# Optimization experiments

Measured on AMD Instinct MI355X. Metric: run time of the kernel, lower is better.

The kernel has to match this reference:

```python
import jax, jax.numpy as jnp
import numpy as np

D_MODEL = 1024
N_HEADS = 16
HEAD_DIM = D_MODEL // N_HEADS


def setup_inputs() -> dict:
    key = jax.random.key(0)
    ks = jax.random.split(key, 5)
    B, T = 4, 4096
    x = jax.random.normal(ks[0], (B, T, D_MODEL), dtype=jnp.float32)
    s = 1.0 / np.sqrt(D_MODEL)
    Wqkv = jax.random.normal(ks[1], (D_MODEL, 3 * D_MODEL), dtype=jnp.float32) * s
    bqkv = jnp.zeros((3 * D_MODEL,), dtype=jnp.float32)
    Wout = jax.random.normal(ks[2], (D_MODEL, D_MODEL), dtype=jnp.float32) * s
    bout = jnp.zeros((D_MODEL,), dtype=jnp.float32)
    return {"x": x, "Wqkv": Wqkv, "bqkv": bqkv, "Wout": Wout, "bout": bout}


def _feature_map(x):
    # elu(x) + 1  (strictly positive feature map)
    return jax.nn.elu(x) + 1.0


def reference(x, Wqkv, bqkv, Wout, bout):
    B, T, C = x.shape
    H, D = N_HEADS, HEAD_DIM
    qkv = x @ Wqkv + bqkv                      # [B,T,3C]
    qkv = qkv.reshape(B, T, 3, H, D)
    qkv = jnp.transpose(qkv, (2, 0, 3, 1, 4))  # [3,B,H,T,D]
    q, k, v = qkv[0], qkv[1], qkv[2]
    scale = D ** 0.25
    q_m = _feature_map(q / scale)
    k_m = _feature_map(k / scale)
    kv = jnp.einsum('bhtd,bhtm->bhdm', k_m, v)     # [B,H,D,D]
    out = jnp.einsum('bhtd,bhdm->bhtm', q_m, kv)   # [B,H,T,D]
    z = q_m.sum(axis=-1, keepdims=True)            # note: sum over feature dim (as in source)
    out = out / (z + 1e-6)
    out = jnp.transpose(out, (0, 2, 1, 3)).reshape(B, T, C)
    return out @ Wout + bout
```

## Files before the change

### kernel.cpp

```cpp
#include <hip/hip_runtime.h>
#include <hip/hip_bf16.h>
#include <math.h>

#define B_ 4
#define T_ 4096
#define H_ 16
#define D_ 64
#define C_ 1024
#define BT_ (B_*T_)

using short8  = __attribute__((ext_vector_type(8))) short;
using floatx4 = __attribute__((ext_vector_type(4))) float;

__device__ __forceinline__ float feature_map(float x) {
    return x > 0.0f ? x + 1.0f : __expf(x);
}
__device__ __forceinline__ unsigned short f2bf(float x) {
    union { __hip_bfloat16 b; unsigned short u; } c;
    c.b = __float2bfloat16(x);
    return c.u;
}
__device__ __forceinline__ float bf2f(unsigned short u) {
    union { unsigned int u; float f; } c;
    c.u = (unsigned)u << 16;
    return c.f;
}
__device__ __forceinline__ void async16(const void* g, void* l) {
    __builtin_amdgcn_global_load_lds(
        (const __attribute__((address_space(1))) void*)g,
        (__attribute__((address_space(3))) void*)l, 16, 0, 0);
}
__device__ __forceinline__ const char* sel3(const char* a0, const char* a1,
                                            const char* a2, int t) {
    return t == 0 ? a0 : (t == 1 ? a1 : a2);
}

__global__ __launch_bounds__(256)
void convert_x_kernel(const float4* __restrict__ x, ushort* __restrict__ xb)
{
    const size_t i = ((size_t)blockIdx.x * 256 + threadIdx.x) * 2;
    const float4 a = x[i], b = x[i + 1];
    short8 r;
    r[0] = (short)f2bf(a.x); r[1] = (short)f2bf(a.y);
    r[2] = (short)f2bf(a.z); r[3] = (short)f2bf(a.w);
    r[4] = (short)f2bf(b.x); r[5] = (short)f2bf(b.y);
    r[6] = (short)f2bf(b.z); r[7] = (short)f2bf(b.w);
    *reinterpret_cast<short8*>(&xb[i * 4]) = r;
}

__global__ __launch_bounds__(256)
void transpose_bf16_kernel(const float* __restrict__ W, ushort* __restrict__ WT,
                           int K, int N)
{
    __shared__ float t[32][33];
    const int n0 = blockIdx.x * 32, k0 = blockIdx.y * 32;
    const int r = threadIdx.x >> 5, c = threadIdx.x & 31;
    #pragma unroll
    for (int i = 0; i < 4; i++)
        t[r + 8 * i][c] = W[(size_t)(k0 + r + 8 * i) * N + n0 + c];
    __syncthreads();
    #pragma unroll
    for (int i = 0; i < 4; i++)
        WT[(size_t)(n0 + r + 8 * i) * K + k0 + c] = f2bf(t[c][r + 8 * i]);
}

#define BAR()    __builtin_amdgcn_s_barrier()
#define WAITDS() do { asm volatile("s_waitcnt lgkmcnt(0)" ::: "memory"); \
                      __builtin_amdgcn_sched_barrier(0); } while(0)
#define VM6()    do { asm volatile("s_waitcnt vmcnt(6)" ::: "memory"); \
                      __builtin_amdgcn_sched_barrier(0); } while(0)

#define LDA(slot, mf, ks, buf) \
    aR[slot][ks] = *(const short8*)(smem + (buf)*32768 + ((mf)>>2)*16384 + \
                                    aRowB + ((mf)&3)*2048 + cks##ks)
#define LDB(nf, ks, buf) \
    bR[nf][ks] = *(const short8*)(smem + 65536 + (buf)*32768 + ((nf)>>1)*16384 + \
                                  bRowB + ((nf)&1)*2048 + cks##ks)
#define LDA8(MB, BUF) do { \
    LDA(0, MB+0, 0, BUF); LDA(0, MB+0, 1, BUF); \
    LDA(1, MB+1, 0, BUF); LDA(1, MB+1, 1, BUF); \
    LDA(2, MB+2, 0, BUF); LDA(2, MB+2, 1, BUF); \
    LDA(3, MB+3, 0, BUF); LDA(3, MB+3, 1, BUF); } while(0)
#define LDB4(NF, BUF) do { \
    LDB(NF+0, 0, BUF); LDB(NF+0, 1, BUF); \
    LDB(NF+1, 0, BUF); LDB(NF+1, 1, BUF); } while(0)

#define MM(mf, nf, ks, slot) \
    acc[mf][nf] = __builtin_amdgcn_mfma_f32_16x16x32_bf16( \
        aR[slot][ks], bR[nf][ks], acc[mf][nf], 0, 0, 0)
#define MFMAQ(MB, NF) do { \
    MM(MB+0,NF+0,0,0); MM(MB+1,NF+0,0,1); MM(MB+2,NF+0,0,2); MM(MB+3,NF+0,0,3); \
    MM(MB+0,NF+1,0,0); MM(MB+1,NF+1,0,1); MM(MB+2,NF+1,0,2); MM(MB+3,NF+1,0,3); \
    MM(MB+0,NF+0,1,0); MM(MB+1,NF+0,1,1); MM(MB+2,NF+0,1,2); MM(MB+3,NF+0,1,3); \
    MM(MB+0,NF+1,1,0); MM(MB+1,NF+1,1,1); MM(MB+2,NF+1,1,2); MM(MB+3,NF+1,1,3); \
} while(0)

#define STGA(h, G, buf) do { int _g = (G); if (_g >= NTILE*16) _g -= NTILE*16; \
    const char* _b = sel3(Ab0, Ab1, Ab2, _g >> 4); const int _w = (_g & 15) * 128; \
    async16(_b + aOf##h##0 + _w, smem + (buf)*32768 + (h)*16384 + wv*1024); \
    async16(_b + aOf##h##1 + _w, smem + (buf)*32768 + (h)*16384 + 8192 + wv*1024); \
} while(0)
#define STGB(h, G, buf) do { int _g = (G); if (_g >= NTILE*16) _g -= NTILE*16; \
    const char* _b = sel3(Bb0, Bb1, Bb2, _g >> 4); const int _w = (_g & 15) * 128; \
    async16(_b + bOf##h##0 + _w, smem + 65536 + (buf)*32768 + (h)*16384 + wv*1024); \
    async16(_b + bOf##h##1 + _w, smem + 65536 + (buf)*32768 + (h)*16384 + 8192 + wv*1024); \
} while(0)

#define ITERBODY(GB) \
    const int g1 = (GB) + 2*it + 1, g2 = (GB) + 2*it + 2, g3 = (GB) + 2*it + 3; \
     LDA8(0, 0); LDB4(0, 0); STGA(1, g1, 1); \
    BAR(); WAITDS(); __builtin_amdgcn_s_setprio(1); MFMAQ(0, 0); \
    __builtin_amdgcn_s_setprio(0); BAR(); \
     LDB4(2, 0); STGA(0, g2, 0); \
    BAR(); WAITDS(); __builtin_amdgcn_s_setprio(1); MFMAQ(0, 2); \
    __builtin_amdgcn_s_setprio(0); BAR(); \
     LDA8(4, 0); STGB(0, g2, 0); \
    BAR(); WAITDS(); __builtin_amdgcn_s_setprio(1); MFMAQ(4, 2); \
    __builtin_amdgcn_s_setprio(0); BAR(); \
     STGB(1, g2, 0); \
    BAR(); WAITDS(); __builtin_amdgcn_s_setprio(1); MFMAQ(4, 0); \
    __builtin_amdgcn_s_setprio(0); VM6(); BAR(); \
     LDA8(0, 1); LDB4(0, 1); STGA(1, g2, 0); \
    BAR(); WAITDS(); __builtin_amdgcn_s_setprio(1); MFMAQ(0, 0); \
    __builtin_amdgcn_s_setprio(0); BAR(); \
     LDB4(2, 1); STGA(0, g3, 1); \
    BAR(); WAITDS(); __builtin_amdgcn_s_setprio(1); MFMAQ(0, 2); \
    __builtin_amdgcn_s_setprio(0); BAR(); \
     LDA8(4, 1); STGB(0, g3, 1); \
    BAR(); WAITDS(); __builtin_amdgcn_s_setprio(1); MFMAQ(4, 2); \
    __builtin_amdgcn_s_setprio(0); BAR(); \
     STGB(1, g3, 1); \
    BAR(); WAITDS(); __builtin_amdgcn_s_setprio(1); MFMAQ(4, 0); \
    __builtin_amdgcn_s_setprio(0); VM6(); BAR();

template<int EPI>
__device__ __forceinline__ void gemm_epilogue(
    floatx4 (&acc)[8][4], const float (&bv)[4],
    int mBase, int nBase, int wm, int wn, int lr, int quad,
    ushort* __restrict__ q_out, ushort* __restrict__ kT_out,
    ushort* __restrict__ vT_out, float* __restrict__ f_out)
{
    if (EPI == 0) {
        const float inv_scale = 0.35355339059327373f;
        const int seg = nBase >> 10;
        if (seg == 0) {
            #pragma unroll
            for (int nf = 0; nf < 4; nf++) {
                const int c = nBase + wn * 64 + nf * 16 + lr;
                #pragma unroll
                for (int mf = 0; mf < 8; mf++)
                    #pragma unroll
                    for (int i = 0; i < 4; i++) {
                        const int t = mBase + wm * 128 + mf * 16 + quad * 4 + i;
                        q_out[(size_t)t * C_ + c] =
                            f2bf(feature_map((acc[mf][nf][i] + bv[nf]) * inv_scale));
                    }
            }
        } else {
            ushort* dstT = (seg == 1) ? kT_out : vT_out;
            #pragma unroll
            for (int nf = 0; nf < 4; nf++) {
                const int c = (nBase + wn * 64 + nf * 16 + lr) & 1023;
                #pragma unroll
                for (int mf = 0; mf < 8; mf++) {
                    float v0 = acc[mf][nf][0] + bv[nf], v1 = acc[mf][nf][1] + bv[nf];
                    float v2 = acc[mf][nf][2] + bv[nf], v3 = acc[mf][nf][3] + bv[nf];
                    if (seg == 1) {
                        v0 = feature_map(v0 * inv_scale); v1 = feature_map(v1 * inv_scale);
                        v2 = feature_map(v2 * inv_scale); v3 = feature_map(v3 * inv_scale);
                    }
                    const int tt = mBase + wm * 128 + mf * 16 + quad * 4;
                    *(ushort4*)&dstT[(size_t)c * BT_ + tt] =
                        make_ushort4(f2bf(v0), f2bf(v1), f2bf(v2), f2bf(v3));
                }
            }
        }
    } else {
        #pragma unroll
        for (int nf = 0; nf < 4; nf++) {
            const int c = nBase + wn * 64 + nf * 16 + lr;
            #pragma unroll
            for (int mf = 0; mf < 8; mf++)
                #pragma unroll
                for (int i = 0; i < 4; i++) {
                    const int row = mBase + wm * 128 + mf * 16 + quad * 4 + i;
                    f_out[(size_t)row * C_ + c] = acc[mf][nf][i] + bv[nf];
                }
        }
    }
    #pragma unroll
    for (int i = 0; i < 8; i++)
        #pragma unroll
        for (int j = 0; j < 4; j++) acc[i][j] = (floatx4)0.0f;
}

template<int EPI, int NBX, int NTILE>
__global__ __launch_bounds__(512, 2)
void gemm256_8ph(const ushort* __restrict__ A, const ushort* __restrict__ Bm,
                 const float* __restrict__ bias,
                 ushort* __restrict__ q_out, ushort* __restrict__ kT_out,
                 ushort* __restrict__ vT_out, float* __restrict__ f_out)
{
    __shared__ __align__(16) unsigned char smem[131072];

    const int tid = threadIdx.x;
    const int wv = tid >> 6, l = tid & 63;
    const int wm = wv >> 2, wn = wv & 3;
    const int lr = l & 15, quad = l >> 4;

    int mB0, mB1, mB2, nB0, nB1, nB2;
    {
        const int tot = (int)gridDim.x * NTILE, cpx = tot >> 3;
        int lg0 = blockIdx.x;
        int w0 = (lg0 & 7) * cpx + (lg0 >> 3);
        mB0 = (w0 / NBX) * 256; nB0 = (w0 % NBX) * 256;
        if (NTILE > 1) {
            int lg1 = blockIdx.x + (int)gridDim.x;
            int w1 = (lg1 & 7) * cpx + (lg1 >> 3);
            mB1 = (w1 / NBX) * 256; nB1 = (w1 % NBX) * 256;
            int lg2 = blockIdx.x + 2 * (int)gridDim.x;
            int w2 = (lg2 & 7) * cpx + (lg2 >> 3);
            mB2 = (w2 / NBX) * 256; nB2 = (w2 % NBX) * 256;
        } else { mB1 = mB0; nB1 = nB0; mB2 = mB0; nB2 = nB0; }
    }
    const char* Ab0 = (const char*)(A + (size_t)mB0 * C_);
    const char* Ab1 = (const char*)(A + (size_t)mB1 * C_);
    const char* Ab2 = (const char*)(A + (size_t)mB2 * C_);
    const char* Bb0 = (const char*)(Bm + (size_t)nB0 * C_);
    const char* Bb1 = (const char*)(Bm + (size_t)nB1 * C_);
    const char* Bb2 = (const char*)(Bm + (size_t)nB2 * C_);

    float bv0[4], bv1[4], bv2[4];
    #pragma unroll
    for (int nf = 0; nf < 4; nf++) {
        bv0[nf] = bias[nB0 + wn * 64 + nf * 16 + lr];
        bv1[nf] = (NTILE > 1) ? bias[nB1 + wn * 64 + nf * 16 + lr] : bv0[nf];
        bv2[nf] = (NTILE > 1) ? bias[nB2 + wn * 64 + nf * 16 + lr] : bv0[nf];
    }

    const int s0 = tid >> 3;
    const int cb = ((tid & 7) * 16) ^ ((s0 & 7) << 4);
    const int aOf00 = (s0)       * 2048 + cb;
    const int aOf01 = (128 + s0) * 2048 + cb;
    const int aOf10 = (64 + s0)  * 2048 + cb;
    const int aOf11 = (192 + s0) * 2048 + cb;
    const int bq    = (s0 >> 5) * 64 + (s0 & 31);
    const int bOf00 = (bq)       * 2048 + cb;
    const int bOf01 = (bq + 128) * 2048 + cb;
    const int bOf10 = (bq + 32)  * 2048 + cb;
    const int bOf11 = (bq + 160) * 2048 + cb;

    const int aRowB = (wm * 64 + lr) * 128;
    const int bRowB = (wn * 32 + lr) * 128;
    const int cks0 = (quad * 16) ^ ((lr & 7) << 4);
    const int cks1 = 64 ^ cks0;

    floatx4 acc[8][4];
    #pragma unroll
    for (int i = 0; i < 8; i++)
        #pragma unroll
        for (int j = 0; j < 4; j++) acc[i][j] = (floatx4)0.0f;
    short8 aR[4][2], bR[4][2];

    STGA(0, 0, 0);
    STGB(0, 0, 0);
    STGB(1, 0, 0);
    STGA(1, 0, 0);
    STGA(0, 1, 1);
    STGB(0, 1, 1);
    STGB(1, 1, 1);
    asm volatile("s_waitcnt vmcnt(6)" ::: "memory");
    __builtin_amdgcn_sched_barrier(0);
    BAR();

    #pragma unroll 1
    for (int it = 0; it < 8; ++it) { ITERBODY(0) }
    gemm_epilogue<EPI>(acc, bv0, mB0, nB0, wm, wn, lr, quad,
                       q_out, kT_out, vT_out, f_out);
    if (NTILE > 1) {
        #pragma unroll 1
        for (int it = 0; it < 8; ++it) { ITERBODY(16) }
        gemm_epilogue<EPI>(acc, bv1, mB1, nB1, wm, wn, lr, quad,
                           q_out, kT_out, vT_out, f_out);
        #pragma unroll 1
        for (int it = 0; it < 8; ++it) { ITERBODY(32) }
        gemm_epilogue<EPI>(acc, bv2, mB2, nB2, wm, wn, lr, quad,
                           q_out, kT_out, vT_out, f_out);
    }
    asm volatile("s_waitcnt vmcnt(0)" ::: "memory");
}

__global__ __launch_bounds__(256)
void kv_accum_kernel(const ushort* __restrict__ kmT, const ushort* __restrict__ vT,
                     float* __restrict__ kv)
{
    const int tid = threadIdx.x;
    const int w = tid >> 6, l = tid & 63;
    const int wm = w >> 1, wn = w & 1;
    const int lr = l & 15, quad = l >> 4;
    const int bh = blockIdx.y;
    const int b = bh >> 4, h = bh & 15;
    const size_t t0 = (size_t)b * T_ + (size_t)blockIdx.x * 512;

    const ushort* Ar = kmT + (size_t)(h * 64 + wm * 32 + lr) * BT_ + t0 + quad * 8;
    const ushort* Br = vT  + (size_t)(h * 64 + wn * 32 + lr) * BT_ + t0 + quad * 8;

    floatx4 acc[2][2];
    #pragma unroll
    for (int i = 0; i < 2; i++)
        #pragma unroll
        for (int j = 0; j < 2; j++) acc[i][j] = (floatx4)0.0f;

    #pragma unroll 8
    for (int tt = 0; tt < 512; tt += 32) {
        const short8 af0 = *(const short8*)&Ar[tt];
        const short8 af1 = *(const short8*)&Ar[(size_t)16 * BT_ + tt];
        const short8 bf0 = *(const short8*)&Br[tt];
        const short8 bf1 = *(const short8*)&Br[(size_t)16 * BT_ + tt];
        acc[0][0] = __builtin_amdgcn_mfma_f32_16x16x32_bf16(af0, bf0, acc[0][0], 0, 0, 0);
        acc[0][1] = __builtin_amdgcn_mfma_f32_16x16x32_bf16(af0, bf1, acc[0][1], 0, 0, 0);
        acc[1][0] = __builtin_amdgcn_mfma_f32_16x16x32_bf16(af1, bf0, acc[1][0], 0, 0, 0);
        acc[1][1] = __builtin_amdgcn_mfma_f32_16x16x32_bf16(af1, bf1, acc[1][1], 0, 0, 0);
    }

    float* kvb = kv + (size_t)bh * (D_ * D_);
    #pragma unroll
    for (int i = 0; i < 2; i++)
        #pragma unroll
        for (int j = 0; j < 2; j++)
            #pragma unroll
            for (int r = 0; r < 4; r++) {
                const int d = wm * 32 + i * 16 + quad * 4 + r;
                const int m = wn * 32 + j * 16 + lr;
                atomicAdd(&kvb[d * 64 + m], acc[i][j][r]);
            }
}

__global__ __launch_bounds__(256)
void pv_kernel(const ushort* __restrict__ qm, const float* __restrict__ kv,
               ushort* __restrict__ attn)
{
    __shared__ ushort kvs[64 * 72];
    const int tid = threadIdx.x;
    const int w = tid >> 6, l = tid & 63;
    const int lr = l & 15, quad = l >> 4;
    const int h = blockIdx.x;
    const int tBase = blockIdx.y * 256;
    const int b = tBase >> 12;

    const float* kvg = kv + ((size_t)b * H_ + h) * (D_ * D_);
    #pragma unroll
    for (int e = 0; e < 4; e++) {
        const int flat = (e * 256 + tid) * 4;
        const float4 vv = *(const float4*)&kvg[flat];
        const int d = flat >> 6, m = flat & 63;
        kvs[(m + 0) * 72 + d] = f2bf(vv.x);
        kvs[(m + 1) * 72 + d] = f2bf(vv.y);
        kvs[(m + 2) * 72 + d] = f2bf(vv.z);
        kvs[(m + 3) * 72 + d] = f2bf(vv.w);
    }
    __syncthreads();

    const int tw = tBase + w * 64;

    floatx4 acc[4][4];
    #pragma unroll
    for (int i = 0; i < 4; i++)
        #pragma unroll
        for (int j = 0; j < 4; j++) acc[i][j] = (floatx4)0.0f;

    float zp[4] = {0.0f, 0.0f, 0.0f, 0.0f};

    #pragma unroll
    for (int kk = 0; kk < 2; kk++) {
        short8 bf[4];
        #pragma unroll
        for (int tf = 0; tf < 4; tf++) {
            bf[tf] = *(const short8*)&qm[(size_t)(tw + tf * 16 + lr) * C_
                                         + h * 64 + kk * 32 + quad * 8];
            #pragma unroll
            for (int j = 0; j < 8; j++) zp[tf] += bf2f((unsigned short)bf[tf][j]);
        }
        short8 af[4];
        #pragma unroll
        for (int mf = 0; mf < 4; mf++)
            af[mf] = *(const short8*)&kvs[(mf * 16 + lr) * 72 + kk * 32 + quad * 8];
        #pragma unroll
        for (int mf = 0; mf < 4; mf++)
            #pragma unroll
            for (int tf = 0; tf < 4; tf++)
                acc[mf][tf] = __builtin_amdgcn_mfma_f32_16x16x32_bf16(
                    af[mf], bf[tf], acc[mf][tf], 0, 0, 0);
    }

    #pragma unroll
    for (int tf = 0; tf < 4; tf++) {
        zp[tf] += __shfl_xor(zp[tf], 16);
        zp[tf] += __shfl_xor(zp[tf], 32);
    }

    #pragma unroll
    for (int tf = 0; tf < 4; tf++) {
        const int t = tw + tf * 16 + lr;
        const float inv = 1.0f / (zp[tf] + 1e-6f);
        #pragma unroll
        for (int mf = 0; mf < 4; mf++) {
            const int m = mf * 16 + quad * 4;
            *(ushort4*)&attn[(size_t)t * C_ + h * 64 + m] =
                make_ushort4(f2bf(acc[mf][tf][0] * inv), f2bf(acc[mf][tf][1] * inv),
                             f2bf(acc[mf][tf][2] * inv), f2bf(acc[mf][tf][3] * inv));
        }
    }
}

extern "C" void kernel_launch(void* const* d_in, const int* in_sizes, int n_in,
                              void* d_out, int out_size, void* d_ws, size_t ws_size,
                              hipStream_t stream)
{
    const float* x    = (const float*)d_in[0];
    const float* Wqkv = (const float*)d_in[1];
    const float* bqkv = (const float*)d_in[2];
    const float* Wout = (const float*)d_in[3];
    const float* bout = (const float*)d_in[4];
    float* out = (float*)d_out;

    char* ws = (char*)d_ws;
    ushort* xb     = (ushort*)ws;
    ushort* WqkvT  = (ushort*)(ws + 33554432);
    ushort* WoutT  = (ushort*)(ws + 39845888);
    ushort* vT     = (ushort*)(ws + 41943040);
    float*  kv     = (float*) (ws + 75497472);
    ushort* attn   = (ushort*)ws;
    ushort* qm     = (ushort*)d_out;
    ushort* kmT    = (ushort*)((char*)d_out + 33554432);

    hipMemsetAsync(kv, 0, (size_t)B_ * H_ * D_ * D_ * sizeof(float), stream);

    convert_x_kernel<<<(BT_ * C_ / 8) / 256, 256, 0, stream>>>((const float4*)x, xb);
    transpose_bf16_kernel<<<dim3(3 * C_ / 32, C_ / 32), 256, 0, stream>>>(Wqkv, WqkvT, C_, 3 * C_);
    transpose_bf16_kernel<<<dim3(C_ / 32, C_ / 32), 256, 0, stream>>>(Wout, WoutT, C_, C_);

    gemm256_8ph<0, 12, 3><<<dim3(256), 512, 0, stream>>>(
        xb, WqkvT, bqkv, qm, kmT, vT, nullptr);
    kv_accum_kernel<<<dim3(8, B_ * H_), 256, 0, stream>>>(kmT, vT, kv);
    pv_kernel<<<dim3(H_, BT_ / 256), 256, 0, stream>>>(qm, kv, attn);
    gemm256_8ph<1, 4, 1><<<dim3(256), 512, 0, stream>>>(
        attn, WoutT, bout, nullptr, nullptr, nullptr, out);
}
```

Baseline: 312.1 us.

## Fold KV state into output projection weights, drop separate attention pass

The normalizer z is computed and applied in the QKV GEMM epilogue, so q is stored pre-scaled. A small per-batch kernel then multiplies each head's KV matrix into Wout, giving a per-batch fused weight. The output GEMM uses q directly against that weight, which removes the pv_kernel and its full read and write of the attention activations. The cost is a per-batch 1024x1024 weight (4x the weight traffic in the out GEMM), extra shuffles in the epilogue, and bf16 rounding of the combined KV·Wout product. The x conversion kernel also switches to a grid-stride loop over 2048 blocks.

```diff
diff --git a/kernel.cpp b/kernel.cpp
--- a/kernel.cpp
+++ b/kernel.cpp
@@ -20,11 +20,6 @@
     c.b = __float2bfloat16(x);
     return c.u;
 }
-__device__ __forceinline__ float bf2f(unsigned short u) {
-    union { unsigned int u; float f; } c;
-    c.u = (unsigned)u << 16;
-    return c.f;
-}
 __device__ __forceinline__ void async16(const void* g, void* l) {
     __builtin_amdgcn_global_load_lds(
         (const __attribute__((address_space(1))) void*)g,
@@ -38,14 +33,17 @@
 __global__ __launch_bounds__(256)
 void convert_x_kernel(const float4* __restrict__ x, ushort* __restrict__ xb)
 {
-    const size_t i = ((size_t)blockIdx.x * 256 + threadIdx.x) * 2;
-    const float4 a = x[i], b = x[i + 1];
-    short8 r;
-    r[0] = (short)f2bf(a.x); r[1] = (short)f2bf(a.y);
-    r[2] = (short)f2bf(a.z); r[3] = (short)f2bf(a.w);
-    r[4] = (short)f2bf(b.x); r[5] = (short)f2bf(b.y);
-    r[6] = (short)f2bf(b.z); r[7] = (short)f2bf(b.w);
-    *reinterpret_cast<short8*>(&xb[i * 4]) = r;
+    const size_t n = (size_t)BT_ * C_ / 8;
+    for (size_t i = (size_t)blockIdx.x * 256 + threadIdx.x; i < n;
+         i += (size_t)2048 * 256) {
+        const float4 a = x[2 * i], b = x[2 * i + 1];
+        short8 r;
+        r[0] = (short)f2bf(a.x); r[1] = (short)f2bf(a.y);
+        r[2] = (short)f2bf(a.z); r[3] = (short)f2bf(a.w);
+        r[4] = (short)f2bf(b.x); r[5] = (short)f2bf(b.y);
+        r[6] = (short)f2bf(b.z); r[7] = (short)f2bf(b.w);
+        *reinterpret_cast<short8*>(&xb[i * 8]) = r;
+    }
 }
 
 __global__ __launch_bounds__(256)
@@ -145,17 +143,24 @@
         const int seg = nBase >> 10;
         if (seg == 0) {
             #pragma unroll
-            for (int nf = 0; nf < 4; nf++) {
-                const int c = nBase + wn * 64 + nf * 16 + lr;
+            for (int mf = 0; mf < 8; mf++)
                 #pragma unroll
-                for (int mf = 0; mf < 8; mf++)
-                    #pragma unroll
-                    for (int i = 0; i < 4; i++) {
-                        const int t = mBase + wm * 128 + mf * 16 + quad * 4 + i;
-                        q_out[(size_t)t * C_ + c] =
-                            f2bf(feature_map((acc[mf][nf][i] + bv[nf]) * inv_scale));
-                    }
-            }
+                for (int i = 0; i < 4; i++) {
+                    float f0 = feature_map((acc[mf][0][i] + bv[0]) * inv_scale);
+                    float f1 = feature_map((acc[mf][1][i] + bv[1]) * inv_scale);
+                    float f2 = feature_map((acc[mf][2][i] + bv[2]) * inv_scale);
+                    float f3 = feature_map((acc[mf][3][i] + bv[3]) * inv_scale);
+                    float z = f0 + f1 + f2 + f3;
+                    z += __shfl_xor(z, 1); z += __shfl_xor(z, 2);
+                    z += __shfl_xor(z, 4); z += __shfl_xor(z, 8);
+                    const float inv = 1.0f / (z + 1e-6f);
+                    const int t = mBase + wm * 128 + mf * 16 + quad * 4 + i;
+                    const int cbase = nBase + wn * 64 + lr;
+                    q_out[(size_t)t * C_ + cbase]      = f2bf(f0 * inv);
+                    q_out[(size_t)t * C_ + cbase + 16] = f2bf(f1 * inv);
+                    q_out[(size_t)t * C_ + cbase + 32] = f2bf(f2 * inv);
+                    q_out[(size_t)t * C_ + cbase + 48] = f2bf(f3 * inv);
+                }
         } else {
             ushort* dstT = (seg == 1) ? kT_out : vT_out;
             #pragma unroll
@@ -195,11 +200,11 @@
 }
 
 template<int EPI, int NBX, int NTILE>
-__global__ __launch_bounds__(512, 2)
-void gemm256_8ph(const ushort* __restrict__ A, const ushort* __restrict__ Bm,
-                 const float* __restrict__ bias,
-                 ushort* __restrict__ q_out, ushort* __restrict__ kT_out,
-                 ushort* __restrict__ vT_out, float* __restrict__ f_out)
+__device__ __forceinline__ void gemm_body(
+    const ushort* __restrict__ A, const ushort* __restrict__ Bm,
+    const float* __restrict__ bias,
+    ushort* __restrict__ q_out, ushort* __restrict__ kT_out,
+    ushort* __restrict__ vT_out, float* __restrict__ f_out)
 {
     __shared__ __align__(16) unsigned char smem[131072];
 
@@ -223,12 +228,13 @@
             mB2 = (w2 / NBX) * 256; nB2 = (w2 % NBX) * 256;
         } else { mB1 = mB0; nB1 = nB0; mB2 = mB0; nB2 = nB0; }
     }
+    const size_t bOffB = (EPI == 1) ? (size_t)(mB0 >> 12) * ((size_t)C_ * C_) : 0;
     const char* Ab0 = (const char*)(A + (size_t)mB0 * C_);
     const char* Ab1 = (const char*)(A + (size_t)mB1 * C_);
     const char* Ab2 = (const char*)(A + (size_t)mB2 * C_);
-    const char* Bb0 = (const char*)(Bm + (size_t)nB0 * C_);
-    const char* Bb1 = (const char*)(Bm + (size_t)nB1 * C_);
-    const char* Bb2 = (const char*)(Bm + (size_t)nB2 * C_);
+    const char* Bb0 = (const char*)(Bm + bOffB + (size_t)nB0 * C_);
+    const char* Bb1 = (const char*)(Bm + bOffB + (size_t)nB1 * C_);
+    const char* Bb2 = (const char*)(Bm + bOffB + (size_t)nB2 * C_);
 
     float bv0[4], bv1[4], bv2[4];
     #pragma unroll
@@ -262,13 +268,8 @@
         for (int j = 0; j < 4; j++) acc[i][j] = (floatx4)0.0f;
     short8 aR[4][2], bR[4][2];
 
-    STGA(0, 0, 0);
-    STGB(0, 0, 0);
-    STGB(1, 0, 0);
-    STGA(1, 0, 0);
-    STGA(0, 1, 1);
-    STGB(0, 1, 1);
-    STGB(1, 1, 1);
+    STGA(0, 0, 0); STGB(0, 0, 0); STGB(1, 0, 0); STGA(1, 0, 0);
+    STGA(0, 1, 1); STGB(0, 1, 1); STGB(1, 1, 1);
     asm volatile("s_waitcnt vmcnt(6)" ::: "memory");
     __builtin_amdgcn_sched_barrier(0);
     BAR();
@@ -290,6 +291,21 @@
     asm volatile("s_waitcnt vmcnt(0)" ::: "memory");
 }
 
+__global__ __launch_bounds__(512, 2)
+void qkv8_kernel(const ushort* __restrict__ A, const ushort* __restrict__ Bm,
+                 const float* __restrict__ bias, ushort* __restrict__ q_out,
+                 ushort* __restrict__ kT_out, ushort* __restrict__ vT_out)
+{
+    gemm_body<0, 12, 3>(A, Bm, bias, q_out, kT_out, vT_out, nullptr);
+}
+
+__global__ __launch_bounds__(512, 2)
+void outproj8_kernel(const ushort* __restrict__ A, const ushort* __restrict__ Bm,
+                     const float* __restrict__ bias, float* __restrict__ f_out)
+{
+    gemm_body<1, 4, 1>(A, Bm, bias, nullptr, nullptr, nullptr, f_out);
+}
+
 __global__ __launch_bounds__(256)
 void kv_accum_kernel(const ushort* __restrict__ kmT, const ushort* __restrict__ vT,
                      float* __restrict__ kv)
@@ -337,31 +353,32 @@
 }
 
 __global__ __launch_bounds__(256)
-void pv_kernel(const ushort* __restrict__ qm, const float* __restrict__ kv,
-               ushort* __restrict__ attn)
-{
-    __shared__ ushort kvs[64 * 72];
+void kw_kernel(const float* __restrict__ kv, const ushort* __restrict__ WoutT,
+               ushort* __restrict__ KWT)
+{
     const int tid = threadIdx.x;
     const int w = tid >> 6, l = tid & 63;
     const int lr = l & 15, quad = l >> 4;
-    const int h = blockIdx.x;
-    const int tBase = blockIdx.y * 256;
-    const int b = tBase >> 12;
-
-    const float* kvg = kv + ((size_t)b * H_ + h) * (D_ * D_);
-    #pragma unroll
-    for (int e = 0; e < 4; e++) {
-        const int flat = (e * 256 + tid) * 4;
-        const float4 vv = *(const float4*)&kvg[flat];
-        const int d = flat >> 6, m = flat & 63;
-        kvs[(m + 0) * 72 + d] = f2bf(vv.x);
-        kvs[(m + 1) * 72 + d] = f2bf(vv.y);
-        kvs[(m + 2) * 72 + d] = f2bf(vv.z);
-        kvs[(m + 3) * 72 + d] = f2bf(vv.w);
-    }
-    __syncthreads();
-
-    const int tw = tBase + w * 64;
+    const int bh = blockIdx.y, b = bh >> 4, h = bh & 15;
+    const int c0 = blockIdx.x * 256 + w * 64;
+
+    const float* kvb = kv + (size_t)bh * (D_ * D_);
+
+    short8 bf[4][2];
+    #pragma unroll
+    for (int df = 0; df < 4; df++)
+        #pragma unroll
+        for (int ks = 0; ks < 2; ks++) {
+            const float* src = &kvb[(df * 16 + lr) * 64 + ks * 32 + quad * 8];
+            const float4 u0 = *(const float4*)src;
+            const float4 u1 = *(const float4*)(src + 4);
+            short8 t;
+            t[0] = (short)f2bf(u0.x); t[1] = (short)f2bf(u0.y);
+            t[2] = (short)f2bf(u0.z); t[3] = (short)f2bf(u0.w);
+            t[4] = (short)f2bf(u1.x); t[5] = (short)f2bf(u1.y);
+            t[6] = (short)f2bf(u1.z); t[7] = (short)f2bf(u1.w);
+            bf[df][ks] = t;
+        }
 
     floatx4 acc[4][4];
     #pragma unroll
@@ -369,48 +386,31 @@
         #pragma unroll
         for (int j = 0; j < 4; j++) acc[i][j] = (floatx4)0.0f;
 
-    float zp[4] = {0.0f, 0.0f, 0.0f, 0.0f};
-
-    #pragma unroll
-    for (int kk = 0; kk < 2; kk++) {
-        short8 bf[4];
-        #pragma unroll
-        for (int tf = 0; tf < 4; tf++) {
-            bf[tf] = *(const short8*)&qm[(size_t)(tw + tf * 16 + lr) * C_
-                                         + h * 64 + kk * 32 + quad * 8];
-            #pragma unroll
-            for (int j = 0; j < 8; j++) zp[tf] += bf2f((unsigned short)bf[tf][j]);
+    #pragma unroll
+    for (int ks = 0; ks < 2; ks++) {
+        short8 af[4];
+        #pragma unroll
+        for (int cf = 0; cf < 4; cf++)
+            af[cf] = *(const short8*)&WoutT[(size_t)(c0 + cf * 16 + lr) * C_
+                                            + h * 64 + ks * 32 + quad * 8];
+        #pragma unroll
+        for (int cf = 0; cf < 4; cf++)
+            #pragma unroll
+            for (int df = 0; df < 4; df++)
+                acc[cf][df] = __builtin_amdgcn_mfma_f32_16x16x32_bf16(
+                    af[cf], bf[df][ks], acc[cf][df], 0, 0, 0);
+    }
+
+    ushort* dst = KWT + (size_t)b * (C_ * C_);
+    #pragma unroll
+    for (int cf = 0; cf < 4; cf++)
+        #pragma unroll
+        for (int i = 0; i < 4; i++) {
+            const int c = c0 + cf * 16 + quad * 4 + i;
+            #pragma unroll
+            for (int df = 0; df < 4; df++)
+                dst[(size_t)c * C_ + h * 64 + df * 16 + lr] = f2bf(acc[cf][df][i]);
         }
-        short8 af[4];
-        #pragma unroll
-        for (int mf = 0; mf < 4; mf++)
-            af[mf] = *(const short8*)&kvs[(mf * 16 + lr) * 72 + kk * 32 + quad * 8];
-        #pragma unroll
-        for (int mf = 0; mf < 4; mf++)
-            #pragma unroll
-            for (int tf = 0; tf < 4; tf++)
-                acc[mf][tf] = __builtin_amdgcn_mfma_f32_16x16x32_bf16(
-                    af[mf], bf[tf], acc[mf][tf], 0, 0, 0);
-    }
-
-    #pragma unroll
-    for (int tf = 0; tf < 4; tf++) {
-        zp[tf] += __shfl_xor(zp[tf], 16);
-        zp[tf] += __shfl_xor(zp[tf], 32);
-    }
-
-    #pragma unroll
-    for (int tf = 0; tf < 4; tf++) {
-        const int t = tw + tf * 16 + lr;
-        const float inv = 1.0f / (zp[tf] + 1e-6f);
-        #pragma unroll
-        for (int mf = 0; mf < 4; mf++) {
-            const int m = mf * 16 + quad * 4;
-            *(ushort4*)&attn[(size_t)t * C_ + h * 64 + m] =
-                make_ushort4(f2bf(acc[mf][tf][0] * inv), f2bf(acc[mf][tf][1] * inv),
-                             f2bf(acc[mf][tf][2] * inv), f2bf(acc[mf][tf][3] * inv));
-        }
-    }
 }
 
 extern "C" void kernel_launch(void* const* d_in, const int* in_sizes, int n_in,
@@ -428,22 +428,20 @@
     ushort* xb     = (ushort*)ws;
     ushort* WqkvT  = (ushort*)(ws + 33554432);
     ushort* WoutT  = (ushort*)(ws + 39845888);
-    ushort* vT     = (ushort*)(ws + 41943040);
+    ushort* qs     = (ushort*)(ws + 41943040);
     float*  kv     = (float*) (ws + 75497472);
-    ushort* attn   = (ushort*)ws;
-    ushort* qm     = (ushort*)d_out;
-    ushort* kmT    = (ushort*)((char*)d_out + 33554432);
+    ushort* KWT    = (ushort*)ws;
+    ushort* kmT    = (ushort*)d_out;
+    ushort* vT     = (ushort*)((char*)d_out + 33554432);
 
     hipMemsetAsync(kv, 0, (size_t)B_ * H_ * D_ * D_ * sizeof(float), stream);
 
-    convert_x_kernel<<<(BT_ * C_ / 8) / 256, 256, 0, stream>>>((const float4*)x, xb);
+    convert_x_kernel<<<2048, 256, 0, stream>>>((const float4*)x, xb);
     transpose_bf16_kernel<<<dim3(3 * C_ / 32, C_ / 32), 256, 0, stream>>>(Wqkv, WqkvT, C_, 3 * C_);
     transpose_bf16_kernel<<<dim3(C_ / 32, C_ / 32), 256, 0, stream>>>(Wout, WoutT, C_, C_);
 
-    gemm256_8ph<0, 12, 3><<<dim3(256), 512, 0, stream>>>(
-        xb, WqkvT, bqkv, qm, kmT, vT, nullptr);
+    qkv8_kernel<<<dim3(256), 512, 0, stream>>>(xb, WqkvT, bqkv, qs, kmT, vT);
     kv_accum_kernel<<<dim3(8, B_ * H_), 256, 0, stream>>>(kmT, vT, kv);
-    pv_kernel<<<dim3(H_, BT_ / 256), 256, 0, stream>>>(qm, kv, attn);
-    gemm256_8ph<1, 4, 1><<<dim3(256), 512, 0, stream>>>(
-        attn, WoutT, bout, nullptr, nullptr, nullptr, out);
-}
+    kw_kernel<<<dim3(4, B_ * H_), 256, 0, stream>>>(kv, WoutT, KWT);
+    outproj8_kernel<<<dim3(256), 512, 0, stream>>>(qs, KWT, bout, out);
+}
```

New measurement: 307.8 us. Within noise of the previous version (-1.4%).
